# Optimization experiments

Hardware: AMD Instinct MI355X
Metric: run time of the kernel (lower is better)

## Reference

```python
import jax, jax.numpy as jnp
import numpy as np

N, C, H, W = 32, 1, 512, 1024
SAMPLE_NUM = 5000
SIGMA = 0.03
ALPHA = 1.0
EPS = 1e-6
LOSS_WEIGHT = 1.0


def setup_inputs() -> dict:
    key = jax.random.key(0)
    k0, k1, k2, k3 = jax.random.split(key, 4)
    prediction = jax.random.normal(k0, (N, C, H, W), dtype=jnp.float32)
    # depths strictly > 0 so target > mask_value (=-1e-8) holds for every pixel,
    # matching the common case where all pixels are 'effective'.
    target = jax.random.uniform(k1, (N, C, H, W), dtype=jnp.float32,
                                minval=0.1, maxval=10.0)
    mask = jax.random.randint(k2, (N, C, H, W), 0, 2).astype(bool)
    # per-image random permutation of pixel indices -> disjoint pairs (A, B),
    # reproducing torch.randperm-based pair sampling as constant indices.
    perm = jax.vmap(lambda k: jax.random.permutation(k, H * W))(
        jax.random.split(k3, N))                      # [N, H*W] int32
    idx_A = perm[:, 0:2 * SAMPLE_NUM:2]               # [N, S]
    idx_B = perm[:, 1:2 * SAMPLE_NUM:2]               # [N, S]
    return {"prediction": prediction, "target": target, "mask": mask,
            "idx_A": idx_A, "idx_B": idx_B}


def reference(prediction, target, mask, idx_A, idx_B):
    n = target.shape[0]
    p = prediction.reshape(n, -1)   # [N, H*W]
    t = target.reshape(n, -1)
    m = mask.reshape(n, -1)

    iA = jnp.take_along_axis(p, idx_A, axis=1)   # [N, S]
    iB = jnp.take_along_axis(p, idx_B, axis=1)
    tA = jnp.take_along_axis(t, idx_A, axis=1)
    tB = jnp.take_along_axis(t, idx_B, axis=1)
    mA = jnp.take_along_axis(m, idx_A, axis=1)
    mB = jnpp_take(m, idx_B) if False else jnp.take_along_axis(m, idx_B, axis=1)

    ratio = tA / (tB + EPS)
    hi = 1.0 + SIGMA
    lo = 1.0 / (1.0 + SIGMA)
    mask_eq = (ratio < hi) & (ratio > lo)
    labels = jnp.where(ratio >= hi, 1.0,
                       jnp.where(ratio <= lo, -1.0, 0.0)).astype(p.dtype)
    cmask = mA & mB

    eq_sel = mask_eq & cmask
    uneq_sel = (~mask_eq) & cmask

    equal_loss = jnp.where(eq_sel, (iA - iB) ** 2, 0.0).sum()
    unequal_loss = jnp.where(
        uneq_sel, jnp.log1p(jnp.exp((iB - iA) * labels)), 0.0).sum()
    valid_samples = cmask.sum().astype(p.dtype)

    loss = (ALPHA * equal_loss + unequal_loss) / (valid_samples + EPS)
    return loss * LOSS_WEIGHT
```

## Files before the change

### kernel.cpp

```cpp
#include <hip/hip_runtime.h>
#include <math.h>

#define SAMPLE_NUM 5000
#define HWSZ (512 * 1024)
#define SIGMA_F 0.03f
#define EPS_F 1e-6f
#define BLOCK 256


template <bool MASK_I32>
__device__ __forceinline__ void
pair_body(const float* __restrict__ pred, const float* __restrict__ targ,
          const void* __restrict__ mask_raw, const int* __restrict__ idxA,
          const int* __restrict__ idxB, int total, float& eq_sum,
          float& uneq_sum, float& valid) {
  const float hi = 1.0f + SIGMA_F;
  const float lo = 1.0f / (1.0f + SIGMA_F);
  const int* m32 = (const int*)mask_raw;
  const unsigned char* m8 = (const unsigned char*)mask_raw;

  const int i = blockIdx.x * BLOCK + threadIdx.x;
  if (i >= total) return;

  const int n = i / SAMPLE_NUM;
  const int base = n * HWSZ;
  const int a = idxA[i];
  const int b = idxB[i];
  const int ia_off = base + a;
  const int ib_off = base + b;

  const int ma = MASK_I32 ? m32[ia_off] : (int)m8[ia_off];
  const int mb = MASK_I32 ? m32[ib_off] : (int)m8[ib_off];

  if (ma && mb) {
    const float tA = targ[ia_off];
    const float tB = targ[ib_off];
    const float iA = pred[ia_off];
    const float iB = pred[ib_off];

    valid += 1.0f;
    const float ratio = tA / (tB + EPS_F);
    if (ratio < hi && ratio > lo) {
      const float d = iA - iB;
      eq_sum += d * d;
    } else {
      const float label = (ratio >= hi) ? 1.0f : -1.0f;
      const float x = (iB - iA) * label;
      uneq_sum += (x > 20.0f) ? x : log1pf(expf(x));
    }
  }
}

__global__ void __launch_bounds__(BLOCK)
ranking_loss_partial(const float* __restrict__ pred,
                     const float* __restrict__ targ,
                     const void* __restrict__ mask_raw,
                     const int* __restrict__ idxA,
                     const int* __restrict__ idxB,
                     float* __restrict__ ws, int total) {
  const unsigned int* mw = (const unsigned int*)mask_raw;
  bool mask_is_i32 = true;
  #pragma unroll
  for (int w = 0; w < 32; ++w) {
    if (mw[w] > 1u) mask_is_i32 = false;
  }

  float eq_sum = 0.0f, uneq_sum = 0.0f, valid = 0.0f;
  if (mask_is_i32) {
    pair_body<true>(pred, targ, mask_raw, idxA, idxB, total, eq_sum, uneq_sum,
                    valid);
  } else {
    pair_body<false>(pred, targ, mask_raw, idxA, idxB, total, eq_sum, uneq_sum,
                     valid);
  }

  #pragma unroll
  for (int off = 32; off > 0; off >>= 1) {
    eq_sum   += __shfl_down(eq_sum, off, 64);
    uneq_sum += __shfl_down(uneq_sum, off, 64);
    valid    += __shfl_down(valid, off, 64);
  }

  __shared__ float s_eq[4], s_un[4], s_va[4];
  const int lane = threadIdx.x & 63;
  const int wave = threadIdx.x >> 6;
  if (lane == 0) {
    s_eq[wave] = eq_sum;
    s_un[wave] = uneq_sum;
    s_va[wave] = valid;
  }
  __syncthreads();

  if (threadIdx.x == 0) {
    float e = 0.0f, u = 0.0f, v = 0.0f;
    #pragma unroll
    for (int w = 0; w < BLOCK / 64; ++w) {
      e += s_eq[w];
      u += s_un[w];
      v += s_va[w];
    }
    float* slot = ws + 3 * blockIdx.x;
    slot[0] = e;
    slot[1] = u;
    slot[2] = v;
  }
}

__global__ void __launch_bounds__(BLOCK)
ranking_loss_finalize(const float* __restrict__ ws, float* __restrict__ out,
                      int nblocks) {
  float e = 0.0f, u = 0.0f, v = 0.0f;
  for (int s = threadIdx.x; s < nblocks; s += BLOCK) {
    e += ws[3 * s + 0];
    u += ws[3 * s + 1];
    v += ws[3 * s + 2];
  }
  #pragma unroll
  for (int off = 32; off > 0; off >>= 1) {
    e += __shfl_down(e, off, 64);
    u += __shfl_down(u, off, 64);
    v += __shfl_down(v, off, 64);
  }
  __shared__ float s_e[4], s_u[4], s_v[4];
  const int lane = threadIdx.x & 63;
  const int wave = threadIdx.x >> 6;
  if (lane == 0) {
    s_e[wave] = e;
    s_u[wave] = u;
    s_v[wave] = v;
  }
  __syncthreads();
  if (threadIdx.x == 0) {
    float te = 0.0f, tu = 0.0f, tv = 0.0f;
    #pragma unroll
    for (int w = 0; w < BLOCK / 64; ++w) {
      te += s_e[w];
      tu += s_u[w];
      tv += s_v[w];
    }
    out[0] = (te + tu) / (tv + EPS_F);
  }
}

extern "C" void kernel_launch(void* const* d_in, const int* in_sizes, int n_in,
                              void* d_out, int out_size, void* d_ws,
                              size_t ws_size, hipStream_t stream) {
  const float* pred = (const float*)d_in[0];
  const float* targ = (const float*)d_in[1];
  const void* mask = d_in[2];
  const int* idxA = (const int*)d_in[3];
  const int* idxB = (const int*)d_in[4];
  float* out = (float*)d_out;
  float* ws = (float*)d_ws;

  const int total = in_sizes[3];
  const int grid = (total + BLOCK - 1) / BLOCK;

  ranking_loss_partial<<<grid, BLOCK, 0, stream>>>(pred, targ, mask, idxA,
                                                   idxB, ws, total);
  ranking_loss_finalize<<<1, BLOCK, 0, stream>>>(ws, out, grid);
}
```

Before: 171.1 us.

## Pack mask into bitmask in a pre-pass before gathering pairs

Adds a kernel that streams the full mask once and packs it into a 1-bit-per-pixel bitmask in workspace. It handles both int32 and byte layouts. The pair kernel then gathers mask bits from this compact array, which should stay cache-resident, instead of doing scattered reads of the original mask. The trade-off is an extra launch and a full sequential read of the mask, even though only a few pixels per image are sampled.

New measurement: 178.6 us. +4.4%, slower.

```diff
diff --git a/kernel.cpp b/kernel.cpp
--- a/kernel.cpp
+++ b/kernel.cpp
@@ -6,58 +6,13 @@
 #define SIGMA_F 0.03f
 #define EPS_F 1e-6f
 #define BLOCK 256
+#define NTOT 32
+#define PACK_WORDS16 (NTOT * HWSZ / 16)
 
 
-template <bool MASK_I32>
-__device__ __forceinline__ void
-pair_body(const float* __restrict__ pred, const float* __restrict__ targ,
-          const void* __restrict__ mask_raw, const int* __restrict__ idxA,
-          const int* __restrict__ idxB, int total, float& eq_sum,
-          float& uneq_sum, float& valid) {
-  const float hi = 1.0f + SIGMA_F;
-  const float lo = 1.0f / (1.0f + SIGMA_F);
-  const int* m32 = (const int*)mask_raw;
-  const unsigned char* m8 = (const unsigned char*)mask_raw;
-
-  const int i = blockIdx.x * BLOCK + threadIdx.x;
-  if (i >= total) return;
-
-  const int n = i / SAMPLE_NUM;
-  const int base = n * HWSZ;
-  const int a = idxA[i];
-  const int b = idxB[i];
-  const int ia_off = base + a;
-  const int ib_off = base + b;
-
-  const int ma = MASK_I32 ? m32[ia_off] : (int)m8[ia_off];
-  const int mb = MASK_I32 ? m32[ib_off] : (int)m8[ib_off];
-
-  if (ma && mb) {
-    const float tA = targ[ia_off];
-    const float tB = targ[ib_off];
-    const float iA = pred[ia_off];
-    const float iB = pred[ib_off];
-
-    valid += 1.0f;
-    const float ratio = tA / (tB + EPS_F);
-    if (ratio < hi && ratio > lo) {
-      const float d = iA - iB;
-      eq_sum += d * d;
-    } else {
-      const float label = (ratio >= hi) ? 1.0f : -1.0f;
-      const float x = (iB - iA) * label;
-      uneq_sum += (x > 20.0f) ? x : log1pf(expf(x));
-    }
-  }
-}
-
 __global__ void __launch_bounds__(BLOCK)
-ranking_loss_partial(const float* __restrict__ pred,
-                     const float* __restrict__ targ,
-                     const void* __restrict__ mask_raw,
-                     const int* __restrict__ idxA,
-                     const int* __restrict__ idxB,
-                     float* __restrict__ ws, int total) {
+mask_pack(const void* __restrict__ mask_raw,
+          unsigned short* __restrict__ out) {
   const unsigned int* mw = (const unsigned int*)mask_raw;
   bool mask_is_i32 = true;
   #pragma unroll
@@ -65,13 +20,69 @@
     if (mw[w] > 1u) mask_is_i32 = false;
   }
 
+  const int i = blockIdx.x * BLOCK + threadIdx.x;
+  if (i >= PACK_WORDS16) return;
+
+  unsigned short r;
+  if (mask_is_i32) {
+    const int* m32 = (const int*)mask_raw;
+    const int b = i * 16;
+    unsigned v = 0;
+    #pragma unroll
+    for (int k = 0; k < 16; ++k) v |= (unsigned)(m32[b + k] & 1) << k;
+    r = (unsigned short)v;
+  } else {
+    const uint4 v = ((const uint4*)mask_raw)[i];
+    const unsigned n0 = ((v.x & 0x01010101u) * 0x01020408u) >> 24;
+    const unsigned n1 = ((v.y & 0x01010101u) * 0x01020408u) >> 24;
+    const unsigned n2 = ((v.z & 0x01010101u) * 0x01020408u) >> 24;
+    const unsigned n3 = ((v.w & 0x01010101u) * 0x01020408u) >> 24;
+    r = (unsigned short)((n0 & 0xFu) | ((n1 & 0xFu) << 4) |
+                         ((n2 & 0xFu) << 8) | ((n3 & 0xFu) << 12));
+  }
+  out[i] = r;
+}
+
+__global__ void __launch_bounds__(BLOCK)
+ranking_loss_partial(const float* __restrict__ pred,
+                     const float* __restrict__ targ,
+                     const unsigned int* __restrict__ mpacked,
+                     const int* __restrict__ idxA,
+                     const int* __restrict__ idxB,
+                     float* __restrict__ ws, int total) {
+  const float hi = 1.0f + SIGMA_F;
+  const float lo = 1.0f / (1.0f + SIGMA_F);
+
   float eq_sum = 0.0f, uneq_sum = 0.0f, valid = 0.0f;
-  if (mask_is_i32) {
-    pair_body<true>(pred, targ, mask_raw, idxA, idxB, total, eq_sum, uneq_sum,
-                    valid);
-  } else {
-    pair_body<false>(pred, targ, mask_raw, idxA, idxB, total, eq_sum, uneq_sum,
-                     valid);
+  const int i = blockIdx.x * BLOCK + threadIdx.x;
+  if (i < total) {
+    const int n = i / SAMPLE_NUM;
+    const int base = n * HWSZ;
+    const int a = idxA[i];
+    const int b = idxB[i];
+    const int ia_off = base + a;
+    const int ib_off = base + b;
+
+    const unsigned wa = mpacked[ia_off >> 5];
+    const unsigned wb = mpacked[ib_off >> 5];
+
+    if ((wa >> (ia_off & 31)) & (wb >> (ib_off & 31)) & 1u) {
+      const float tA = targ[ia_off];
+      const float tB = targ[ib_off];
+      const float iA = pred[ia_off];
+      const float iB = pred[ib_off];
+
+      valid += 1.0f;
+      const float ratio = tA / (tB + EPS_F);
+      if (ratio < hi && ratio > lo) {
+        const float d = iA - iB;
+        eq_sum += d * d;
+      } else {
+        const float label = (ratio >= hi) ? 1.0f : -1.0f;
+        const float x = (iB - iA) * label;
+        uneq_sum += (x > 20.0f) ? x : log1pf(expf(x));
+      }
+    }
   }
 
   #pragma unroll
@@ -156,7 +167,11 @@
   const int total = in_sizes[3];
   const int grid = (total + BLOCK - 1) / BLOCK;
 
-  ranking_loss_partial<<<grid, BLOCK, 0, stream>>>(pred, targ, mask, idxA,
+  unsigned short* mpack16 = (unsigned short*)((char*)d_ws + 8192);
+  const unsigned int* mpack32 = (const unsigned int*)mpack16;
+
+  mask_pack<<<PACK_WORDS16 / BLOCK, BLOCK, 0, stream>>>(mask, mpack16);
+  ranking_loss_partial<<<grid, BLOCK, 0, stream>>>(pred, targ, mpack32, idxA,
                                                    idxB, ws, total);
   ranking_loss_finalize<<<1, BLOCK, 0, stream>>>(ws, out, grid);
 }
```
